# Optimization experiments

Measured on AMD Instinct MI355X. Metric: run time of the kernel, lower is better.

## Reference

```python
import jax, jax.numpy as jnp
import numpy as np

B, H, FEAT = 16384, 256, 256
GX, GY, SW = 70, 70, 2


def setup_inputs() -> dict:
    key = jax.random.key(0)
    ks = jax.random.split(key, 10)
    stdv = 1.0 / np.sqrt(H)
    feats = jax.random.normal(ks[0], (B, FEAT), dtype=jnp.float32)
    coords = jax.random.randint(ks[1], (B, 2), 0, 64).astype(jnp.float32)
    input_tensor = jnp.concatenate([feats, coords], axis=1)  # [B, FEAT+2]
    hidden = jax.random.normal(ks[2], (B, H), dtype=jnp.float32)
    u = lambda k, shp: jax.random.uniform(k, shp, jnp.float32, -stdv, stdv)
    return {
        "input_tensor": input_tensor,
        "hidden": hidden,
        "w_ih": u(ks[3], (4 * H, FEAT)),
        "b_ih": u(ks[4], (4 * H,)),
        "w_hh": u(ks[5], (4 * H, H)),
        "b_hh": u(ks[6], (4 * H,)),
        "w_out": u(ks[7], (H, 2 * H)),
        "b_out": u(ks[8], (H,)),
        "memory": jax.random.normal(ks[9], (GX, GY, H), dtype=jnp.float32) * 0.1,
    }


def reference(input_tensor, hidden, w_ih, b_ih, w_hh, b_hh, w_out, b_out, memory):
    feature = input_tensor[:, :-2]
    grid = input_tensor[:, -2:].astype(jnp.int32) + SW  # [B,2]

    gi = feature @ w_ih.T + b_ih  # [B,4H]
    gh = hidden @ w_hh.T + b_hh   # [B,4H]
    i_r, i_i, i_n, i_s = jnp.split(gi, 4, axis=1)
    h_r, h_i, h_n, h_s = jnp.split(gh, 4, axis=1)

    resetgate = jax.nn.sigmoid(i_r + h_r)
    updategate = jax.nn.sigmoid(i_i + h_i)
    spatialgate = jax.nn.sigmoid(i_s + h_s)
    newgate = jnp.tanh(i_n + resetgate * h_n)

    # gather (2*SW+1)^2 neighborhood per sample from spatial memory
    gx = jnp.clip(grid[:, 0], 0, GX - 1)
    gy = jnp.clip(grid[:, 1], 0, GY - 1)
    off = jnp.arange(-SW, SW + 1)  # [K]
    xi = jnp.clip(gx[:, None] + off[None, :], 0, GX - 1)  # [B,K]
    yi = jnp.clip(gy[:, None] + off[None, :], 0, GY - 1)  # [B,K]
    K = 2 * SW + 1
    x_flat = jnp.broadcast_to(xi[:, :, None], (xi.shape[0], K, K)).reshape(xi.shape[0], -1)
    y_flat = jnp.broadcast_to(yi[:, None, :], (yi.shape[0], K, K)).reshape(yi.shape[0], -1)
    context = memory[x_flat, y_flat]  # [B, K*K, H]

    # attention (query is detached in original)
    q = jax.lax.stop_gradient(newgate)  # [B,H]
    attn = jnp.einsum('bh,bkh->bk', q, context)  # [B, K*K]
    attn = jnp.where(attn == 0, -jnp.inf, attn)
    w = jax.nn.softmax(attn, axis=1)
    w = jnp.where(jnp.isnan(w), 0.0, w)
    mix = jnp.einsum('bk,bkh->bh', w, context)  # [B,H]
    combined = jnp.concatenate([mix, q], axis=1)  # [B,2H]
    atten_cs = jnp.tanh(combined @ w_out.T + b_out)  # [B,H]

    curr_state = newgate + spatialgate * atten_cs
    output = curr_state + updategate * (hidden - curr_state)
    return output
```

## Files before the change

### kernel.cpp

```cpp
#include <hip/hip_runtime.h>
#include <stdint.h>

#define B_N 16384
#define H_N 256
#define IN_W 258
#define GX_N 70
#define GY_N 70
#define SW_N 2
#define KK_N 25

typedef __bf16 bf16x8 __attribute__((ext_vector_type(8)));
typedef __bf16 bf16x4 __attribute__((ext_vector_type(4)));
typedef __bf16 bf16x2 __attribute__((ext_vector_type(2)));
typedef float f32x4 __attribute__((ext_vector_type(4)));

#define AS1 __attribute__((address_space(1)))
#define AS3 __attribute__((address_space(3)))

static __device__ __forceinline__ void gload16(const void* g, void* l) {
    __builtin_amdgcn_global_load_lds((const AS1 uint32_t*)g, (AS3 uint32_t*)l, 16, 0, 0);
}

#define E_AB   8388608ULL
#define E_WF   8912896ULL
#define E_WOUT 9043968ULL
#define E_COMB 9043968ULL
#define E_UGSG 17432576ULL

__global__ __launch_bounds__(256) void cast_kernel(
    const float* __restrict__ in_t, const float* __restrict__ hid,
    const float* __restrict__ wih, const float* __restrict__ whh,
    const float* __restrict__ wout, __bf16* __restrict__ dst)
{
    size_t g = (size_t)blockIdx.x * blockDim.x + threadIdx.x;
    size_t stride = (size_t)gridDim.x * blockDim.x;
    for (size_t e = g * 4; e < E_WOUT; e += stride * 4) {
        const float* src;
        if (e < E_AB) {
            size_t row = e >> 9;
            size_t c = e & 511;
            src = (c < 256) ? (in_t + row * IN_W + c) : (hid + row * 256 + (c - 256));
        } else if (e < E_WF) {
            size_t off = e - E_AB;
            size_t j = off >> 9;
            size_t k = off & 511;
            size_t c = j >> 8;
            size_t col = j & 255;
            size_t base = (c == 0) ? 0 : (c == 1) ? 256 : (c == 2) ? 768 : 512;
            const float* srcm = (k < 256) ? wih : whh;
            src = srcm + (base + col) * 256 + (k & 255);
        } else {
            src = wout + (e - E_WF);
        }
        bf16x4 o;
        o.x = (__bf16)src[0];
        o.y = (__bf16)src[1];
        o.z = (__bf16)src[2];
        o.w = (__bf16)src[3];
        *reinterpret_cast<bf16x4*>(dst + e) = o;
    }
}

__global__ __launch_bounds__(256, 3) void gates_gemm(
    const __bf16* __restrict__ AB, const __bf16* __restrict__ wfull,
    const float* __restrict__ b_ih, const float* __restrict__ b_hh,
    __bf16* __restrict__ comb, __bf16* __restrict__ ugsg)
{
    __shared__ __bf16 ldsA[4096], ldsB[4096];
    const int t = threadIdx.x;
    const int lane = t & 63, w = t >> 6;
    const int lr = lane & 15, seg = lane >> 4;
    const int rb = blockIdx.x * 128;
    const int h0 = blockIdx.y * 32;

    const int r_s = t & 127;
    const int s_lo = t >> 7;
    const __bf16* gA = AB + (size_t)(rb + r_s) * 512 + s_lo * 8;
    const int wr = ((r_s >> 5) << 8) + h0 + (r_s & 31);
    const __bf16* gB = wfull + (size_t)wr * 512 + s_lo * 8;
    __bf16* lA = ldsA + t * 8;
    __bf16* lB = ldsB + t * 8;

    f32x4 acc_s[3][2][2], acc_ni[2][2], acc_nh[2][2];
#pragma unroll
    for (int hh = 0; hh < 2; hh++)
#pragma unroll
        for (int rh = 0; rh < 2; rh++) {
#pragma unroll
            for (int c = 0; c < 3; c++) acc_s[c][hh][rh] = (f32x4){0.f, 0.f, 0.f, 0.f};
            acc_ni[hh][rh] = (f32x4){0.f, 0.f, 0.f, 0.f};
            acc_nh[hh][rh] = (f32x4){0.f, 0.f, 0.f, 0.f};
        }

#pragma unroll 1
    for (int half = 0; half < 2; half++) {
        for (int kt = half * 256; kt < half * 256 + 256; kt += 32) {
            gload16(gA + kt, lA);
            gload16(gA + kt + 16, lA + 2048);
            gload16(gB + kt, lB);
            gload16(gB + kt + 16, lB + 2048);
            __syncthreads();

            bf16x8 af[2];
#pragma unroll
            for (int rh = 0; rh < 2; rh++) {
                int tr = w * 32 + rh * 16 + lr;
                af[rh] = *reinterpret_cast<const bf16x8*>(ldsA + seg * 1024 + tr * 8);
            }
#pragma unroll
            for (int c = 0; c < 4; c++)
#pragma unroll
                for (int hh = 0; hh < 2; hh++) {
                    int br = c * 32 + hh * 16 + lr;
                    bf16x8 bb = *reinterpret_cast<const bf16x8*>(ldsB + seg * 1024 + br * 8);
#pragma unroll
                    for (int rh = 0; rh < 2; rh++) {
                        if (c < 3)
                            acc_s[c][hh][rh] = __builtin_amdgcn_mfma_f32_16x16x32_bf16(af[rh], bb, acc_s[c][hh][rh], 0, 0, 0);
                        else if (half == 0)
                            acc_ni[hh][rh] = __builtin_amdgcn_mfma_f32_16x16x32_bf16(af[rh], bb, acc_ni[hh][rh], 0, 0, 0);
                        else
                            acc_nh[hh][rh] = __builtin_amdgcn_mfma_f32_16x16x32_bf16(af[rh], bb, acc_nh[hh][rh], 0, 0, 0);
                    }
                }
            __syncthreads();
        }
    }

#pragma unroll
    for (int hh = 0; hh < 2; hh++) {
        int col = h0 + hh * 16 + lr;
        float br_ = b_ih[col] + b_hh[col];
        float bi_ = b_ih[col + 256] + b_hh[col + 256];
        float bs_ = b_ih[col + 768] + b_hh[col + 768];
        float bni = b_ih[col + 512];
        float bnh = b_hh[col + 512];
#pragma unroll
        for (int rh = 0; rh < 2; rh++) {
#pragma unroll
            for (int r = 0; r < 4; r++) {
                int row = rb + w * 32 + rh * 16 + seg * 4 + r;
                float sr = acc_s[0][hh][rh][r] + br_;
                float si = acc_s[1][hh][rh][r] + bi_;
                float ss = acc_s[2][hh][rh][r] + bs_;
                float ni = acc_ni[hh][rh][r] + bni;
                float nh = acc_nh[hh][rh][r] + bnh;
                float rg = 1.f / (1.f + __expf(-sr));
                float ug = 1.f / (1.f + __expf(-si));
                float sg = 1.f / (1.f + __expf(-ss));
                float ng = tanhf(ni + rg * nh);
                comb[(size_t)row * 512 + 256 + col] = (__bf16)ng;
                bf16x2 us;
                us.x = (__bf16)ug;
                us.y = (__bf16)sg;
                *reinterpret_cast<bf16x2*>(ugsg + ((size_t)row * 256 + col) * 2) = us;
            }
        }
    }
}

__global__ __launch_bounds__(256) void attn_kernel(
    const float* __restrict__ in_t, const float* __restrict__ memory,
    __bf16* __restrict__ comb)
{
    const int w = threadIdx.x >> 6;
    const int lane = threadIdx.x & 63;
    const int b = blockIdx.x * 4 + w;
    const float* row_in = in_t + (size_t)b * IN_W;
    int gx = (int)row_in[256] + SW_N;
    int gy = (int)row_in[257] + SW_N;
    gx = min(max(gx, 0), GX_N - 1);
    gy = min(max(gy, 0), GY_N - 1);

    bf16x4 qb = *reinterpret_cast<const bf16x4*>(comb + (size_t)b * 512 + 256 + lane * 4);
    float q0 = (float)qb.x, q1 = (float)qb.y, q2 = (float)qb.z, q3 = (float)qb.w;

    float m = -INFINITY, d = 0.f;
    float o0 = 0.f, o1 = 0.f, o2 = 0.f, o3 = 0.f;
#pragma unroll
    for (int k = 0; k < KK_N; k++) {
        int i = k / 5, j = k % 5;
        int xi = min(max(gx + i - SW_N, 0), GX_N - 1);
        int yj = min(max(gy + j - SW_N, 0), GY_N - 1);
        const f32x4* cp = reinterpret_cast<const f32x4*>(memory + ((size_t)xi * GY_N + yj) * H_N);
        f32x4 v = cp[lane];
        float p = q0 * v.x + q1 * v.y + q2 * v.z + q3 * v.w;
        for (int off = 32; off; off >>= 1) p += __shfl_xor(p, off, 64);
        float a = (p == 0.f) ? -INFINITY : p;
        float mn = fmaxf(m, a);
        if (mn != -INFINITY) {
            float alpha = __expf(m - mn);
            float e = __expf(a - mn);
            d = d * alpha + e;
            o0 = o0 * alpha + e * v.x;
            o1 = o1 * alpha + e * v.y;
            o2 = o2 * alpha + e * v.z;
            o3 = o3 * alpha + e * v.w;
            m = mn;
        }
    }
    float inv = (d != 0.f) ? 1.f / d : 0.f;
    bf16x4 ob;
    ob.x = (__bf16)(o0 * inv);
    ob.y = (__bf16)(o1 * inv);
    ob.z = (__bf16)(o2 * inv);
    ob.w = (__bf16)(o3 * inv);
    *reinterpret_cast<bf16x4*>(comb + (size_t)b * 512 + lane * 4) = ob;
}

__global__ __launch_bounds__(256, 4) void out_gemm(
    const __bf16* __restrict__ comb, const __bf16* __restrict__ woB,
    const float* __restrict__ b_out, const __bf16* __restrict__ ugsg,
    const float* __restrict__ hidden, float* __restrict__ out)
{
    __shared__ __bf16 ldsA[4096], ldsB[2048];
    const int t = threadIdx.x;
    const int lane = t & 63, w = t >> 6;
    const int lr = lane & 15, seg = lane >> 4;
    const int rb = blockIdx.x * 128;
    const int n0 = blockIdx.y * 64;

    const int rA = t & 127;
    const int sA = t >> 7;
    const __bf16* gA = comb + (size_t)(rb + rA) * 512 + sA * 8;
    __bf16* lA = ldsA + t * 8;
    const __bf16* gB = woB + (size_t)(n0 + (t & 63)) * 512 + (t >> 6) * 8;
    __bf16* lB = ldsB + t * 8;

    f32x4 acc[2][4];
#pragma unroll
    for (int rh = 0; rh < 2; rh++)
#pragma unroll
        for (int ct = 0; ct < 4; ct++) acc[rh][ct] = (f32x4){0.f, 0.f, 0.f, 0.f};

    for (int kt = 0; kt < 512; kt += 32) {
        gload16(gA + kt, lA);
        gload16(gA + kt + 16, lA + 2048);
        gload16(gB + kt, lB);
        __syncthreads();

        bf16x8 af[2];
#pragma unroll
        for (int rh = 0; rh < 2; rh++) {
            int tr = w * 32 + rh * 16 + lr;
            af[rh] = *reinterpret_cast<const bf16x8*>(ldsA + seg * 1024 + tr * 8);
        }
#pragma unroll
        for (int ct = 0; ct < 4; ct++) {
            bf16x8 bb = *reinterpret_cast<const bf16x8*>(ldsB + seg * 512 + (ct * 16 + lr) * 8);
#pragma unroll
            for (int rh = 0; rh < 2; rh++)
                acc[rh][ct] = __builtin_amdgcn_mfma_f32_16x16x32_bf16(af[rh], bb, acc[rh][ct], 0, 0, 0);
        }
        __syncthreads();
    }

#pragma unroll
    for (int ct = 0; ct < 4; ct++) {
        int col = n0 + ct * 16 + lr;
        float bo = b_out[col];
#pragma unroll
        for (int rh = 0; rh < 2; rh++) {
#pragma unroll
            for (int r = 0; r < 4; r++) {
                int row = rb + w * 32 + rh * 16 + seg * 4 + r;
                size_t idx = (size_t)row * 256 + col;
                float acs = tanhf(acc[rh][ct][r] + bo);
                float ng = (float)comb[(size_t)row * 512 + 256 + col];
                bf16x2 us = *reinterpret_cast<const bf16x2*>(ugsg + idx * 2);
                float ug = (float)us.x, sg = (float)us.y;
                float curr = ng + sg * acs;
                out[idx] = curr + ug * (hidden[idx] - curr);
            }
        }
    }
}

extern "C" void kernel_launch(void* const* d_in, const int* in_sizes, int n_in,
                              void* d_out, int out_size, void* d_ws, size_t ws_size,
                              hipStream_t stream) {
    const float* input_t = (const float*)d_in[0];
    const float* hidden  = (const float*)d_in[1];
    const float* w_ih    = (const float*)d_in[2];
    const float* b_ih    = (const float*)d_in[3];
    const float* w_hh    = (const float*)d_in[4];
    const float* b_hh    = (const float*)d_in[5];
    const float* w_out   = (const float*)d_in[6];
    const float* b_out   = (const float*)d_in[7];
    const float* memory  = (const float*)d_in[8];
    float* out = (float*)d_out;

    __bf16* base  = (__bf16*)d_ws;
    __bf16* AB    = base;
    __bf16* wfull = base + E_AB;
    __bf16* woutB = base + E_WF;
    __bf16* comb  = base + E_COMB;
    __bf16* ugsg  = base + E_UGSG;

    cast_kernel<<<4096, 256, 0, stream>>>(input_t, hidden, w_ih, w_hh, w_out, base);
    gates_gemm<<<dim3(128, 8), 256, 0, stream>>>(AB, wfull, b_ih, b_hh, comb, ugsg);
    attn_kernel<<<4096, 256, 0, stream>>>(input_t, memory, comb);
    out_gemm<<<dim3(128, 4), 256, 0, stream>>>(comb, woutB, b_out, ugsg, hidden, out);
}
```

Before: 209.9 us.

## Double-buffer LDS in both GEMMs and enlarge gates GEMM row tile

```diff
diff --git a/kernel.cpp b/kernel.cpp
--- a/kernel.cpp
+++ b/kernel.cpp
@@ -61,94 +61,114 @@
     }
 }
 
-__global__ __launch_bounds__(256, 3) void gates_gemm(
+__global__ __launch_bounds__(256, 2) void gates_gemm(
     const __bf16* __restrict__ AB, const __bf16* __restrict__ wfull,
     const float* __restrict__ b_ih, const float* __restrict__ b_hh,
     __bf16* __restrict__ comb, __bf16* __restrict__ ugsg)
 {
-    __shared__ __bf16 ldsA[4096], ldsB[4096];
+    __shared__ __bf16 ldsA[2][8192];
+    __shared__ __bf16 ldsB[2][4096];
     const int t = threadIdx.x;
     const int lane = t & 63, w = t >> 6;
     const int lr = lane & 15, seg = lane >> 4;
-    const int rb = blockIdx.x * 128;
+    const int rb = blockIdx.x * 256;
     const int h0 = blockIdx.y * 32;
 
-    const int r_s = t & 127;
-    const int s_lo = t >> 7;
-    const __bf16* gA = AB + (size_t)(rb + r_s) * 512 + s_lo * 8;
-    const int wr = ((r_s >> 5) << 8) + h0 + (r_s & 31);
-    const __bf16* gB = wfull + (size_t)wr * 512 + s_lo * 8;
-    __bf16* lA = ldsA + t * 8;
-    __bf16* lB = ldsB + t * 8;
-
-    f32x4 acc_s[3][2][2], acc_ni[2][2], acc_nh[2][2];
-#pragma unroll
-    for (int hh = 0; hh < 2; hh++)
-#pragma unroll
-        for (int rh = 0; rh < 2; rh++) {
-#pragma unroll
-            for (int c = 0; c < 3; c++) acc_s[c][hh][rh] = (f32x4){0.f, 0.f, 0.f, 0.f};
-            acc_ni[hh][rh] = (f32x4){0.f, 0.f, 0.f, 0.f};
-            acc_nh[hh][rh] = (f32x4){0.f, 0.f, 0.f, 0.f};
-        }
+    const __bf16* gAt = AB + (size_t)(rb + t) * 512;
+    const int bc = (t & 127) >> 5;
+    const int bcol = t & 31;
+    const __bf16* gBt = wfull + (size_t)(bc * 256 + h0 + bcol) * 512 + ((t >> 7) << 3);
+    __bf16* lA0 = &ldsA[0][t * 8];
+    __bf16* lA1 = &ldsA[1][t * 8];
+    __bf16* lB0 = &ldsB[0][t * 8];
+    __bf16* lB1 = &ldsB[1][t * 8];
+
+    f32x4 acc[4][6], accni[4][2], accnh[4][2];
+#pragma unroll
+    for (int rh = 0; rh < 4; rh++) {
+#pragma unroll
+        for (int cn = 0; cn < 6; cn++) acc[rh][cn] = (f32x4){0.f, 0.f, 0.f, 0.f};
+        accni[rh][0] = (f32x4){0.f, 0.f, 0.f, 0.f};
+        accni[rh][1] = (f32x4){0.f, 0.f, 0.f, 0.f};
+        accnh[rh][0] = (f32x4){0.f, 0.f, 0.f, 0.f};
+        accnh[rh][1] = (f32x4){0.f, 0.f, 0.f, 0.f};
+    }
+
+    gload16(gAt + 0, lA0);
+    gload16(gAt + 8, lA0 + 2048);
+    gload16(gAt + 16, lA0 + 4096);
+    gload16(gAt + 24, lA0 + 6144);
+    gload16(gBt + 0, lB0);
+    gload16(gBt + 16, lB0 + 2048);
+    __syncthreads();
 
 #pragma unroll 1
-    for (int half = 0; half < 2; half++) {
-        for (int kt = half * 256; kt < half * 256 + 256; kt += 32) {
-            gload16(gA + kt, lA);
-            gload16(gA + kt + 16, lA + 2048);
-            gload16(gB + kt, lB);
-            gload16(gB + kt + 16, lB + 2048);
-            __syncthreads();
-
-            bf16x8 af[2];
-#pragma unroll
-            for (int rh = 0; rh < 2; rh++) {
-                int tr = w * 32 + rh * 16 + lr;
-                af[rh] = *reinterpret_cast<const bf16x8*>(ldsA + seg * 1024 + tr * 8);
+    for (int tt = 0; tt < 16; tt++) {
+        const int cur = tt & 1;
+        if (tt < 15) {
+            const int kn = (tt + 1) * 32;
+            __bf16* la = cur ? lA0 : lA1;
+            __bf16* lb = cur ? lB0 : lB1;
+            gload16(gAt + kn, la);
+            gload16(gAt + kn + 8, la + 2048);
+            gload16(gAt + kn + 16, la + 4096);
+            gload16(gAt + kn + 24, la + 6144);
+            gload16(gBt + kn, lb);
+            gload16(gBt + kn + 16, lb + 2048);
+        }
+        const __bf16* cA = ldsA[cur];
+        const __bf16* cB = ldsB[cur];
+        bf16x8 af[4];
+#pragma unroll
+        for (int rh = 0; rh < 4; rh++)
+            af[rh] = *reinterpret_cast<const bf16x8*>(cA + seg * 2048 + (w * 64 + rh * 16 + lr) * 8);
+#pragma unroll
+        for (int cn = 0; cn < 6; cn++) {
+            bf16x8 bb = *reinterpret_cast<const bf16x8*>(cB + seg * 1024 + (cn * 16 + lr) * 8);
+#pragma unroll
+            for (int rh = 0; rh < 4; rh++)
+                acc[rh][cn] = __builtin_amdgcn_mfma_f32_16x16x32_bf16(af[rh], bb, acc[rh][cn], 0, 0, 0);
+        }
+        bf16x8 b6 = *reinterpret_cast<const bf16x8*>(cB + seg * 1024 + (96 + lr) * 8);
+        bf16x8 b7 = *reinterpret_cast<const bf16x8*>(cB + seg * 1024 + (112 + lr) * 8);
+        if (tt < 8) {
+#pragma unroll
+            for (int rh = 0; rh < 4; rh++) {
+                accni[rh][0] = __builtin_amdgcn_mfma_f32_16x16x32_bf16(af[rh], b6, accni[rh][0], 0, 0, 0);
+                accni[rh][1] = __builtin_amdgcn_mfma_f32_16x16x32_bf16(af[rh], b7, accni[rh][1], 0, 0, 0);
             }
-#pragma unroll
-            for (int c = 0; c < 4; c++)
-#pragma unroll
-                for (int hh = 0; hh < 2; hh++) {
-                    int br = c * 32 + hh * 16 + lr;
-                    bf16x8 bb = *reinterpret_cast<const bf16x8*>(ldsB + seg * 1024 + br * 8);
-#pragma unroll
-                    for (int rh = 0; rh < 2; rh++) {
-                        if (c < 3)
-                            acc_s[c][hh][rh] = __builtin_amdgcn_mfma_f32_16x16x32_bf16(af[rh], bb, acc_s[c][hh][rh], 0, 0, 0);
-                        else if (half == 0)
-                            acc_ni[hh][rh] = __builtin_amdgcn_mfma_f32_16x16x32_bf16(af[rh], bb, acc_ni[hh][rh], 0, 0, 0);
-                        else
-                            acc_nh[hh][rh] = __builtin_amdgcn_mfma_f32_16x16x32_bf16(af[rh], bb, acc_nh[hh][rh], 0, 0, 0);
-                    }
-                }
-            __syncthreads();
-        }
+        } else {
+#pragma unroll
+            for (int rh = 0; rh < 4; rh++) {
+                accnh[rh][0] = __builtin_amdgcn_mfma_f32_16x16x32_bf16(af[rh], b6, accnh[rh][0], 0, 0, 0);
+                accnh[rh][1] = __builtin_amdgcn_mfma_f32_16x16x32_bf16(af[rh], b7, accnh[rh][1], 0, 0, 0);
+            }
+        }
+        __syncthreads();
     }
 
 #pragma unroll
     for (int hh = 0; hh < 2; hh++) {
-        int col = h0 + hh * 16 + lr;
-        float br_ = b_ih[col] + b_hh[col];
-        float bi_ = b_ih[col + 256] + b_hh[col + 256];
-        float bs_ = b_ih[col + 768] + b_hh[col + 768];
-        float bni = b_ih[col + 512];
-        float bnh = b_hh[col + 512];
-#pragma unroll
-        for (int rh = 0; rh < 2; rh++) {
+        const int col = h0 + hh * 16 + lr;
+        const float br_ = b_ih[col] + b_hh[col];
+        const float bi_ = b_ih[col + 256] + b_hh[col + 256];
+        const float bs_ = b_ih[col + 768] + b_hh[col + 768];
+        const float bni = b_ih[col + 512];
+        const float bnh = b_hh[col + 512];
+#pragma unroll
+        for (int rh = 0; rh < 4; rh++) {
 #pragma unroll
             for (int r = 0; r < 4; r++) {
-                int row = rb + w * 32 + rh * 16 + seg * 4 + r;
-                float sr = acc_s[0][hh][rh][r] + br_;
-                float si = acc_s[1][hh][rh][r] + bi_;
-                float ss = acc_s[2][hh][rh][r] + bs_;
-                float ni = acc_ni[hh][rh][r] + bni;
-                float nh = acc_nh[hh][rh][r] + bnh;
+                const int row = rb + w * 64 + rh * 16 + seg * 4 + r;
+                float sr = acc[rh][hh][r] + br_;
+                float si = acc[rh][2 + hh][r] + bi_;
+                float ss = acc[rh][4 + hh][r] + bs_;
+                float vni = accni[rh][hh][r] + bni;
+                float vnh = accnh[rh][hh][r] + bnh;
                 float rg = 1.f / (1.f + __expf(-sr));
                 float ug = 1.f / (1.f + __expf(-si));
                 float sg = 1.f / (1.f + __expf(-ss));
-                float ng = tanhf(ni + rg * nh);
+                float ng = tanhf(vni + rg * vnh);
                 comb[(size_t)row * 512 + 256 + col] = (__bf16)ng;
                 bf16x2 us;
                 us.x = (__bf16)ug;
@@ -213,19 +233,20 @@
     const float* __restrict__ b_out, const __bf16* __restrict__ ugsg,
     const float* __restrict__ hidden, float* __restrict__ out)
 {
-    __shared__ __bf16 ldsA[4096], ldsB[2048];
+    __shared__ __bf16 ldsA[2][4096];
+    __shared__ __bf16 ldsB[2][2048];
     const int t = threadIdx.x;
     const int lane = t & 63, w = t >> 6;
     const int lr = lane & 15, seg = lane >> 4;
     const int rb = blockIdx.x * 128;
     const int n0 = blockIdx.y * 64;
 
-    const int rA = t & 127;
-    const int sA = t >> 7;
-    const __bf16* gA = comb + (size_t)(rb + rA) * 512 + sA * 8;
-    __bf16* lA = ldsA + t * 8;
-    const __bf16* gB = woB + (size_t)(n0 + (t & 63)) * 512 + (t >> 6) * 8;
-    __bf16* lB = ldsB + t * 8;
+    const __bf16* gAt = comb + (size_t)(rb + (t & 127)) * 512 + ((t >> 7) << 3);
+    const __bf16* gBt = woB + (size_t)(n0 + (t & 63)) * 512 + ((t >> 6) << 3);
+    __bf16* lA0 = &ldsA[0][t * 8];
+    __bf16* lA1 = &ldsA[1][t * 8];
+    __bf16* lB0 = &ldsB[0][t * 8];
+    __bf16* lB1 = &ldsB[1][t * 8];
 
     f32x4 acc[2][4];
 #pragma unroll
@@ -233,21 +254,31 @@
 #pragma unroll
         for (int ct = 0; ct < 4; ct++) acc[rh][ct] = (f32x4){0.f, 0.f, 0.f, 0.f};
 
-    for (int kt = 0; kt < 512; kt += 32) {
-        gload16(gA + kt, lA);
-        gload16(gA + kt + 16, lA + 2048);
-        gload16(gB + kt, lB);
-        __syncthreads();
-
+    gload16(gAt + 0, lA0);
+    gload16(gAt + 16, lA0 + 2048);
+    gload16(gBt + 0, lB0);
+    __syncthreads();
+
+#pragma unroll 1
+    for (int tt = 0; tt < 16; tt++) {
+        const int cur = tt & 1;
+        if (tt < 15) {
+            const int kn = (tt + 1) * 32;
+            __bf16* la = cur ? lA0 : lA1;
+            __bf16* lb = cur ? lB0 : lB1;
+            gload16(gAt + kn, la);
+            gload16(gAt + kn + 16, la + 2048);
+            gload16(gBt + kn, lb);
+        }
+        const __bf16* cA = ldsA[cur];
+        const __bf16* cB = ldsB[cur];
         bf16x8 af[2];
 #pragma unroll
-        for (int rh = 0; rh < 2; rh++) {
-            int tr = w * 32 + rh * 16 + lr;
-            af[rh] = *reinterpret_cast<const bf16x8*>(ldsA + seg * 1024 + tr * 8);
-        }
+        for (int rh = 0; rh < 2; rh++)
+            af[rh] = *reinterpret_cast<const bf16x8*>(cA + seg * 1024 + (w * 32 + rh * 16 + lr) * 8);
 #pragma unroll
         for (int ct = 0; ct < 4; ct++) {
-            bf16x8 bb = *reinterpret_cast<const bf16x8*>(ldsB + seg * 512 + (ct * 16 + lr) * 8);
+            bf16x8 bb = *reinterpret_cast<const bf16x8*>(cB + seg * 512 + (ct * 16 + lr) * 8);
 #pragma unroll
             for (int rh = 0; rh < 2; rh++)
                 acc[rh][ct] = __builtin_amdgcn_mfma_f32_16x16x32_bf16(af[rh], bb, acc[rh][ct], 0, 0, 0);
@@ -298,7 +329,7 @@
     __bf16* ugsg  = base + E_UGSG;
 
     cast_kernel<<<4096, 256, 0, stream>>>(input_t, hidden, w_ih, w_hh, w_out, base);
-    gates_gemm<<<dim3(128, 8), 256, 0, stream>>>(AB, wfull, b_ih, b_hh, comb, ugsg);
+    gates_gemm<<<dim3(64, 8), 256, 0, stream>>>(AB, wfull, b_ih, b_hh, comb, ugsg);
     attn_kernel<<<4096, 256, 0, stream>>>(input_t, memory, comb);
     out_gemm<<<dim3(128, 4), 256, 0, stream>>>(comb, woutB, b_out, ugsg, hidden, out);
 }
```

Result: no change. 205.8 us (-2.0%).
